# Kernel optimization log

Hardware: AMD Instinct MI355X
Metric: run time of the kernel (lower is better)

## Reference

```python
import jax, jax.numpy as jnp
import numpy as np
import math

NEG_INF = -1000000000.0
D_EMBED = 1024
D_K = 1024
N_HEADS = 16
D_H = D_EMBED // N_HEADS


def setup_inputs() -> dict:
    key = jax.random.key(0)
    ks = jax.random.split(key, 12)
    B, S = 2, 2048
    s = 0.02
    return {
        "embed": jax.random.normal(ks[0], (B, S, D_EMBED), dtype=jnp.float32),
        "key": jax.random.normal(ks[1], (B, S, D_K), dtype=jnp.float32),
        "attn_mask": jax.random.randint(ks[2], (B, S, S), 0, 2, dtype=jnp.int32),
        "Wq": jax.random.normal(ks[3], (D_EMBED, D_EMBED), dtype=jnp.float32) * s,
        "bq": jnp.zeros((D_EMBED,), dtype=jnp.float32),
        "Wk": jax.random.normal(ks[4], (D_EMBED, D_K), dtype=jnp.float32) * s,
        "bk": jnp.zeros((D_EMBED,), dtype=jnp.float32),
        "Wv": jax.random.normal(ks[5], (D_EMBED, D_K), dtype=jnp.float32) * s,
        "bv": jnp.zeros((D_EMBED,), dtype=jnp.float32),
        "Wo": jax.random.normal(ks[6], (D_EMBED, D_EMBED), dtype=jnp.float32) * s,
        "bo": jnp.zeros((D_EMBED,), dtype=jnp.float32),
    }


def _alibi_bias(seq_len: int, n_heads: int) -> jnp.ndarray:
    # symmetric |i-j| distances, slopes 2^-(8k/H) for k=1..H
    r = jnp.arange(seq_len)
    pos = jnp.abs(r[None, :] - r[:, None]).astype(jnp.float32)  # [S, S]
    step = 8.0 / n_heads
    ms = 2.0 ** (-jnp.arange(step, 8.0 + step, step, dtype=jnp.float32))  # [H]
    return ms[:, None, None] * pos[None, :, :]  # [H, S, S]


def reference(embed, key, attn_mask, Wq, bq, Wk, bk, Wv, bv, Wo, bo):
    B, Sq, _ = embed.shape
    Sk = key.shape[1]
    Q = embed @ Wq.T + bq          # [B, Sq, D]
    K = key @ Wk.T + bk            # [B, Sk, D]
    V = key @ Wv.T + bv            # [B, Sk, D]
    Qh = Q.reshape(B, Sq, N_HEADS, D_H).transpose(0, 2, 1, 3)  # [B, H, Sq, d_h]
    Kh = K.reshape(B, Sk, N_HEADS, D_H).transpose(0, 2, 1, 3)
    Vh = V.reshape(B, Sk, N_HEADS, D_H).transpose(0, 2, 1, 3)
    attn = jnp.einsum("bhqd,bhkd->bhqk", Qh, Kh)
    # ALiBi bias subtracted BEFORE scaling (as in source)
    attn = attn - _alibi_bias(Sq, N_HEADS)[None]
    attn = attn * (1.0 / math.sqrt(D_EMBED))  # note: scale uses d_embed, not d_h
    attn = jnp.where(attn_mask[:, None, :, :] == 0, NEG_INF, attn)
    attn = jax.nn.softmax(attn, axis=-1)
    out = jnp.einsum("bhqk,bhkd->bhqd", attn, Vh)
    out = out.transpose(0, 2, 1, 3).reshape(B, Sq, D_EMBED)
    return out @ Wo.T + bo
```

## Files before the change

### kernel.cpp

```cpp
#include <hip/hip_runtime.h>


typedef _Float16 f16;
typedef __attribute__((ext_vector_type(8))) _Float16 f16x8;
typedef __attribute__((ext_vector_type(4))) _Float16 f16x4;
typedef __attribute__((ext_vector_type(4))) float f32x4;
typedef unsigned long long u64;
typedef unsigned int u32;

#define MFMA16 __builtin_amdgcn_mfma_f32_16x16x32_f16
#define MFMA16K16 __builtin_amdgcn_mfma_f32_16x16x16f16

__global__ __launch_bounds__(256) void k_convert(
    const float* __restrict__ embed, const float* __restrict__ key,
    const float* __restrict__ wq, const float* __restrict__ wk,
    const float* __restrict__ wv, const float* __restrict__ wo,
    f16* __restrict__ xe, f16* __restrict__ xk,
    f16* __restrict__ wqh, f16* __restrict__ wkh,
    f16* __restrict__ wvh, f16* __restrict__ woh)
{
    long g = (long)blockIdx.x * 256 + threadIdx.x;
    const float* src; f16* dst; long off;
    if (g < 524288)       { src = embed; dst = xe; off = g; }
    else if (g < 1048576) { src = key;   dst = xk; off = g - 524288; }
    else {
        long t = g - 1048576; int wi = (int)(t >> 17); off = t & 131071;
        if (wi == 0)      { src = wq; dst = wqh; }
        else if (wi == 1) { src = wk; dst = wkh; }
        else if (wi == 2) { src = wv; dst = wvh; }
        else              { src = wo; dst = woh; }
    }
    const float4* s4 = (const float4*)src;
    float4 a = s4[off * 2], b = s4[off * 2 + 1];
    f16x8 o;
    o[0]=(f16)a.x; o[1]=(f16)a.y; o[2]=(f16)a.z; o[3]=(f16)a.w;
    o[4]=(f16)b.x; o[5]=(f16)b.y; o[6]=(f16)b.z; o[7]=(f16)b.w;
    *(f16x8*)(dst + off * 8) = o;
}

__global__ __launch_bounds__(256) void k_packmask(
    const int* __restrict__ mask, u64* __restrict__ bits)
{
    int gw = (blockIdx.x * 256 + threadIdx.x) >> 6;
    int lane = threadIdx.x & 63;
    const int* row = mask + (long)gw * 2048;
    u64* out = bits + (long)gw * 32;
    #pragma unroll 4
    for (int c = 0; c < 32; ++c) {
        int v = row[c * 64 + lane];
        u64 b = __ballot(v != 0);
        if (lane == 0) out[c] = b;
    }
}

__global__ __launch_bounds__(256) void k_qkv(
    const f16* __restrict__ xe, const f16* __restrict__ xk,
    const f16* __restrict__ wqh, const f16* __restrict__ wkh, const f16* __restrict__ wvh,
    const float* __restrict__ bq, const float* __restrict__ bk, const float* __restrict__ bv,
    f16* __restrict__ Qh, f16* __restrict__ Kh, f16* __restrict__ Vt)
{
    int bid = blockIdx.x;
    int which = bid >> 8;
    int rr_ = bid & 255;
    int tm = rr_ >> 3, tn = rr_ & 7;
    const f16* X = (which == 0) ? xe : xk;
    const f16* W = (which == 0) ? wqh : (which == 1) ? wkh : wvh;
    const float* bias = (which == 0) ? bq : (which == 1) ? bk : bv;

    __shared__ f16 smem[128 * 136];
    f16* la = smem;
    f16* lb = smem + 128 * 64;

    int tid = threadIdx.x;
    int lane = tid & 63, wid = tid >> 6;
    int wr = wid >> 1, wc = wid & 1;
    int lm = lane & 15, qd = lane >> 4;

    f32x4 acc[4][4];
    #pragma unroll
    for (int i = 0; i < 4; i++)
        #pragma unroll
        for (int j = 0; j < 4; j++) acc[i][j] = (f32x4)0.0f;

    int m0 = tm * 128, n0 = tn * 128;

    for (int kt = 0; kt < 16; ++kt) {
        int k0 = kt * 64;
        __syncthreads();
        #pragma unroll
        for (int t = 0; t < 4; ++t) {
            int cid = tid + t * 256;
            int row = cid >> 3;
            int cg = cid & 7;
            int sw = cg ^ (row & 7);
            *(f16x8*)&la[row * 64 + sw * 8] =
                *(const f16x8*)&X[(long)(m0 + row) * 1024 + k0 + cg * 8];
            *(f16x8*)&lb[row * 64 + sw * 8] =
                *(const f16x8*)&W[(long)(n0 + row) * 1024 + k0 + cg * 8];
        }
        __syncthreads();
        #pragma unroll
        for (int ks = 0; ks < 2; ++ks) {
            f16x8 af[4], bfr[4];
            #pragma unroll
            for (int i = 0; i < 4; i++) {
                int m = 64 * wr + 16 * i + lm;
                int g = (ks * 4 + qd) ^ (m & 7);
                af[i] = *(const f16x8*)&la[m * 64 + g * 8];
                int n = 64 * wc + 16 * i + lm;
                int g2 = (ks * 4 + qd) ^ (n & 7);
                bfr[i] = *(const f16x8*)&lb[n * 64 + g2 * 8];
            }
            #pragma unroll
            for (int i = 0; i < 4; i++)
                #pragma unroll
                for (int j = 0; j < 4; j++)
                    acc[i][j] = MFMA16(af[i], bfr[j], acc[i][j], 0, 0, 0);
        }
    }

    if (which == 2) {
        #pragma unroll
        for (int j = 0; j < 4; j++) {
            int n = n0 + 64 * wc + 16 * j + lm;
            float bb = bias[n];
            int h = n >> 6, d = n & 63;
            #pragma unroll
            for (int i = 0; i < 4; i++) {
                int mbase = m0 + 64 * wr + 16 * i + 4 * qd;
                f16x4 pk;
                #pragma unroll
                for (int r = 0; r < 4; ++r) pk[r] = (f16)(acc[i][j][r] + bb);
                int b = mbase >> 11, s = mbase & 2047;
                *(f16x4*)&Vt[(((long)(b * 16 + h)) * 64 + d) * 2048 + s] = pk;
            }
        }
    } else {
        f16* dst = (which == 0) ? Qh : Kh;
        float sc = (which == 0) ? 0.0450842252f : 1.0f;
        __syncthreads();
        #pragma unroll
        for (int j = 0; j < 4; j++) {
            int col = 64 * wc + 16 * j + lm;
            float bb = bias[n0 + col];
            #pragma unroll
            for (int i = 0; i < 4; i++) {
                int row = 64 * wr + 16 * i + 4 * qd;
                #pragma unroll
                for (int r = 0; r < 4; ++r)
                    smem[(row + r) * 136 + col] = (f16)((acc[i][j][r] + bb) * sc);
            }
        }
        __syncthreads();
        #pragma unroll
        for (int t = 0; t < 8; ++t) {
            int ci = tid + t * 256;
            int row = ci >> 4, cg = ci & 15;
            f16x8 v = *(const f16x8*)&smem[row * 136 + cg * 8];
            int m = m0 + row;
            int b = m >> 11, s = m & 2047;
            int h = (n0 >> 6) + (cg >> 3);
            int d0 = (cg & 7) * 8;
            *(f16x8*)&dst[(((long)(b * 16 + h)) * 2048 + s) * 64 + d0] = v;
        }
    }
}

__global__ __launch_bounds__(256, 2) void k_attn(
    const f16* __restrict__ Qh, const f16* __restrict__ Kh, const f16* __restrict__ Vt,
    const u64* __restrict__ mbits, f16* __restrict__ O)
{
    int bid = blockIdx.x;
    int qt = bid & 15;
    int h = (bid >> 4) & 15;
    int b = bid >> 8;
    int q0 = qt * 128;

    const f16* Qg = Qh + ((long)(b * 16 + h)) * 2048 * 64;
    const f16* Kg = Kh + ((long)(b * 16 + h)) * 2048 * 64;
    const f16* Vg = Vt + ((long)(b * 16 + h)) * 64 * 2048;

    __shared__ f16 ks[128 * 64];
    __shared__ f16 vs[64 * 128];

    int tid = threadIdx.x, lane = tid & 63, wid = tid >> 6;
    int lm = lane & 15, qd = lane >> 4;

    int qb = q0 + 32 * wid;
    const u64* Mrow0 = mbits + ((long)(b * 2048) + qb + lm) * 32;
    const u64* Mrow1 = mbits + ((long)(b * 2048) + qb + 16 + lm) * 32;

    f16x8 aq[2][2];
    #pragma unroll
    for (int g = 0; g < 2; ++g)
        #pragma unroll
        for (int ksi = 0; ksi < 2; ++ksi)
            aq[g][ksi] = *(const f16x8*)&Qg[(long)(qb + 16 * g + lm) * 64 + ksi * 32 + qd * 8];

    f32x4 oacc[2][4], lacc[2];
    #pragma unroll
    for (int g = 0; g < 2; ++g) {
        #pragma unroll
        for (int c = 0; c < 4; c++) oacc[g][c] = (f32x4)0.0f;
        lacc[g] = (f32x4)0.0f;
    }
    f16x4 vone4;
    #pragma unroll
    for (int j = 0; j < 4; j++) vone4[j] = (f16)1.0f;

    float negc2 = -__builtin_amdgcn_exp2f(-0.5f * (float)(h + 1)) * 0.0450842252f;

    for (int kt = 0; kt < 16; ++kt) {
        int k0 = kt * 128;
        __syncthreads();
        #pragma unroll
        for (int t = 0; t < 4; ++t) {
            int cid = tid + t * 256;
            int row = cid >> 3, cg = cid & 7;
            int sw = cg ^ (row & 7);
            *(f16x8*)&ks[row * 64 + sw * 8] =
                *(const f16x8*)&Kg[(long)(k0 + row) * 64 + cg * 8];
            int vrow = cid >> 4, vg = cid & 15;
            int vsw = vg ^ (vrow & 7);
            *(f16x8*)&vs[vrow * 128 + vsw * 8] =
                *(const f16x8*)&Vg[(long)vrow * 2048 + k0 + vg * 8];
        }
        __syncthreads();

        u64 w0a = Mrow0[kt * 2], w1a = Mrow0[kt * 2 + 1];
        u64 w0b = Mrow1[kt * 2], w1b = Mrow1[kt * 2 + 1];

        f32x4 sacc[2][8];
        #pragma unroll
        for (int g = 0; g < 2; ++g)
            #pragma unroll
            for (int c = 0; c < 8; c++) sacc[g][c] = (f32x4)0.0f;
        #pragma unroll
        for (int ksi = 0; ksi < 2; ++ksi) {
            #pragma unroll
            for (int c = 0; c < 8; c++) {
                int kr = 16 * c + lm;
                int gg = (ksi * 4 + qd) ^ (kr & 7);
                f16x8 ak = *(const f16x8*)&ks[kr * 64 + gg * 8];
                sacc[0][c] = MFMA16(ak, aq[0][ksi], sacc[0][c], 0, 0, 0);
                sacc[1][c] = MFMA16(ak, aq[1][ksi], sacc[1][c], 0, 0, 0);
            }
        }

        float qmk0 = (float)(qb + lm - k0 - 4 * qd);
        float qmk1 = qmk0 + 16.0f;
        int shb = 4 * qd;
        int vgq = qd >> 1;
        int off4 = (qd & 1) * 4;
        #pragma unroll
        for (int c = 0; c < 8; c++) {
            u32 niba = (u32)(((c < 4) ? w0a : w1a) >> (16 * (c & 3) + shb)) & 15u;
            u32 nibb = (u32)(((c < 4) ? w0b : w1b) >> (16 * (c & 3) + shb)) & 15u;
            float qc0 = qmk0 - 16.0f * (float)c;
            float qc1 = qmk1 - 16.0f * (float)c;
            f16x4 pk0, pk1;
            #pragma unroll
            for (int r = 0; r < 4; ++r) {
                float u0 = fmaf(fabsf(qc0 - (float)r), negc2, sacc[0][c][r]);
                u0 = ((niba >> r) & 1u) ? u0 : -1e30f;
                pk0[r] = (f16)__builtin_amdgcn_exp2f(u0);
                float u1 = fmaf(fabsf(qc1 - (float)r), negc2, sacc[1][c][r]);
                u1 = ((nibb >> r) & 1u) ? u1 : -1e30f;
                pk1[r] = (f16)__builtin_amdgcn_exp2f(u1);
            }
            int vgc = 2 * c + vgq;
            #pragma unroll
            for (int cc = 0; cc < 4; ++cc) {
                int d = 16 * cc + lm;
                f16x4 vb = *(const f16x4*)&vs[d * 128 + (vgc ^ (d & 7)) * 8 + off4];
                oacc[0][cc] = MFMA16K16(pk0, vb, oacc[0][cc], 0, 0, 0);
                oacc[1][cc] = MFMA16K16(pk1, vb, oacc[1][cc], 0, 0, 0);
            }
            lacc[0] = MFMA16K16(pk0, vone4, lacc[0], 0, 0, 0);
            lacc[1] = MFMA16K16(pk1, vone4, lacc[1], 0, 0, 0);
        }
    }

    #pragma unroll
    for (int g = 0; g < 2; ++g) {
        #pragma unroll
        for (int r = 0; r < 4; ++r) {
            float linv = 1.0f / fmaxf(lacc[g][r], 1e-30f);
            long rowbase = ((long)(b * 2048 + qb + 16 * g + 4 * qd + r)) * 1024 + h * 64;
            #pragma unroll
            for (int cc = 0; cc < 4; ++cc)
                O[rowbase + 16 * cc + lm] = (f16)(oacc[g][cc][r] * linv);
        }
    }
}

__global__ __launch_bounds__(256) void k_proj(
    const f16* __restrict__ Oh, const f16* __restrict__ woh,
    const float* __restrict__ bo, float* __restrict__ out)
{
    int bid = blockIdx.x;
    int tm = bid >> 3, tn = bid & 7;

    __shared__ f16 la[128 * 64];
    __shared__ f16 lb[128 * 64];

    int tid = threadIdx.x;
    int lane = tid & 63, wid = tid >> 6;
    int wr = wid >> 1, wc = wid & 1;
    int lm = lane & 15, qd = lane >> 4;

    f32x4 acc[4][4];
    #pragma unroll
    for (int i = 0; i < 4; i++)
        #pragma unroll
        for (int j = 0; j < 4; j++) acc[i][j] = (f32x4)0.0f;

    int m0 = tm * 128, n0 = tn * 128;

    for (int kt = 0; kt < 16; ++kt) {
        int k0 = kt * 64;
        __syncthreads();
        #pragma unroll
        for (int t = 0; t < 4; ++t) {
            int cid = tid + t * 256;
            int row = cid >> 3;
            int cg = cid & 7;
            int sw = cg ^ (row & 7);
            *(f16x8*)&la[row * 64 + sw * 8] =
                *(const f16x8*)&Oh[(long)(m0 + row) * 1024 + k0 + cg * 8];
            *(f16x8*)&lb[row * 64 + sw * 8] =
                *(const f16x8*)&woh[(long)(n0 + row) * 1024 + k0 + cg * 8];
        }
        __syncthreads();
        #pragma unroll
        for (int ks = 0; ks < 2; ++ks) {
            f16x8 af[4], bfr[4];
            #pragma unroll
            for (int i = 0; i < 4; i++) {
                int m = 64 * wr + 16 * i + lm;
                int g = (ks * 4 + qd) ^ (m & 7);
                af[i] = *(const f16x8*)&la[m * 64 + g * 8];
                int n = 64 * wc + 16 * i + lm;
                int g2 = (ks * 4 + qd) ^ (n & 7);
                bfr[i] = *(const f16x8*)&lb[n * 64 + g2 * 8];
            }
            #pragma unroll
            for (int i = 0; i < 4; i++)
                #pragma unroll
                for (int j = 0; j < 4; j++)
                    acc[i][j] = MFMA16(af[i], bfr[j], acc[i][j], 0, 0, 0);
        }
    }

    #pragma unroll
    for (int j = 0; j < 4; j++) {
        int n = n0 + 64 * wc + 16 * j + lm;
        float bb = bo[n];
        #pragma unroll
        for (int i = 0; i < 4; i++) {
            int mbase = m0 + 64 * wr + 16 * i + 4 * qd;
            #pragma unroll
            for (int r = 0; r < 4; ++r)
                out[(long)(mbase + r) * 1024 + n] = acc[i][j][r] + bb;
        }
    }
}

extern "C" void kernel_launch(void* const* d_in, const int* in_sizes, int n_in,
                              void* d_out, int out_size, void* d_ws, size_t ws_size,
                              hipStream_t stream)
{
    const float* embed = (const float*)d_in[0];
    const float* key   = (const float*)d_in[1];
    const int*   mask  = (const int*)d_in[2];
    const float* Wq = (const float*)d_in[3];
    const float* bq = (const float*)d_in[4];
    const float* Wk = (const float*)d_in[5];
    const float* bk = (const float*)d_in[6];
    const float* Wv = (const float*)d_in[7];
    const float* bv = (const float*)d_in[8];
    const float* Wo = (const float*)d_in[9];
    const float* bo = (const float*)d_in[10];

    char* ws = (char*)d_ws;
    f16* xe  = (f16*)(ws + 0);
    f16* xk  = (f16*)(ws + 8388608);
    f16* wqh = (f16*)(ws + 16777216);
    f16* wkh = (f16*)(ws + 18874368);
    f16* wvh = (f16*)(ws + 20971520);
    f16* woh = (f16*)(ws + 23068672);
    f16* Qh  = (f16*)(ws + 25165824);
    f16* Kh  = (f16*)(ws + 33554432);
    f16* Vt  = (f16*)(ws + 41943040);
    f16* Oh  = (f16*)(ws + 50331648);
    u64* mb  = (u64*)(ws + 58720256);
    float* out = (float*)d_out;

    k_convert<<<6144, 256, 0, stream>>>(embed, key, Wq, Wk, Wv, Wo,
                                        xe, xk, wqh, wkh, wvh, woh);
    k_packmask<<<1024, 256, 0, stream>>>(mask, mb);
    k_qkv<<<768, 256, 0, stream>>>(xe, xk, wqh, wkh, wvh, bq, bk, bv, Qh, Kh, Vt);
    k_attn<<<512, 256, 0, stream>>>(Qh, Kh, Vt, mb, Oh);
    k_proj<<<256, 256, 0, stream>>>(Oh, woh, bo, out);
}
```

Measured before the change: 287.5 us.

## Split attention keys across two wave groups with direct global-to-LDS loads

After: 287.3 us. No clear change (-0.1%).

```diff
diff --git a/kernel.cpp b/kernel.cpp
--- a/kernel.cpp
+++ b/kernel.cpp
@@ -10,6 +10,13 @@
 
 #define MFMA16 __builtin_amdgcn_mfma_f32_16x16x32_f16
 #define MFMA16K16 __builtin_amdgcn_mfma_f32_16x16x16f16
+
+__device__ __forceinline__ void gl16(const f16* g, f16* l) {
+    __builtin_amdgcn_global_load_lds(
+        (const __attribute__((address_space(1))) void*)(const void*)g,
+        (__attribute__((address_space(3))) void*)(void*)l,
+        16, 0, 0);
+}
 
 __global__ __launch_bounds__(256) void k_convert(
     const float* __restrict__ embed, const float* __restrict__ key,
@@ -166,7 +173,7 @@
     }
 }
 
-__global__ __launch_bounds__(256, 2) void k_attn(
+__global__ __launch_bounds__(512, 4) void k_attn(
     const f16* __restrict__ Qh, const f16* __restrict__ Kh, const f16* __restrict__ Vt,
     const u64* __restrict__ mbits, f16* __restrict__ O)
 {
@@ -180,16 +187,39 @@
     const f16* Kg = Kh + ((long)(b * 16 + h)) * 2048 * 64;
     const f16* Vg = Vt + ((long)(b * 16 + h)) * 64 * 2048;
 
-    __shared__ f16 ks[128 * 64];
-    __shared__ f16 vs[64 * 128];
+    __shared__ f16 smem[32768];
 
     int tid = threadIdx.x, lane = tid & 63, wid = tid >> 6;
     int lm = lane & 15, qd = lane >> 4;
-
-    int qb = q0 + 32 * wid;
+    int qs = wid & 3;
+    int hf = wid >> 2;
+
+    int qb = q0 + 32 * qs;
     const u64* Mrow0 = mbits + ((long)(b * 2048) + qb + lm) * 32;
     const u64* Mrow1 = mbits + ((long)(b * 2048) + qb + 16 + lm) * 32;
 
+    int bi = wid >> 1, sub = wid & 1;
+    f16* ldst = smem + bi * 8192 + sub * 4096;
+    const f16* gE; const f16* gO; long gstep;
+    if (bi < 2) {
+        int krow0 = sub * 64 + (lane >> 3);
+        int kcg = (lane & 7) ^ (krow0 & 7);
+        gE = Kg + ((long)bi * 1024 + krow0) * 64 + kcg * 8;
+        gO = gE + 512;
+        gstep = 1024;
+    } else {
+        int vh = bi - 2;
+        int vrow0 = sub * 32 + (lane >> 4);
+        int vgE = (lane & 15) ^ (vrow0 & 7);
+        gE = Vg + (long)vrow0 * 2048 + vh * 1024 + vgE * 8;
+        gO = Vg + (long)(vrow0 + 4) * 2048 + vh * 1024 + (vgE ^ 4) * 8;
+        gstep = 16384;
+    }
+    long giter = (bi < 2) ? (long)128 * 64 : 128;
+
+    const f16* ksH = smem + hf * 8192;
+    const f16* vsH = smem + 16384 + hf * 8192;
+
     f16x8 aq[2][2];
     #pragma unroll
     for (int g = 0; g < 2; ++g)
@@ -210,50 +240,38 @@
 
     float negc2 = -__builtin_amdgcn_exp2f(-0.5f * (float)(h + 1)) * 0.0450842252f;
 
-    for (int kt = 0; kt < 16; ++kt) {
-        int k0 = kt * 128;
-        __syncthreads();
-        #pragma unroll
-        for (int t = 0; t < 4; ++t) {
-            int cid = tid + t * 256;
-            int row = cid >> 3, cg = cid & 7;
-            int sw = cg ^ (row & 7);
-            *(f16x8*)&ks[row * 64 + sw * 8] =
-                *(const f16x8*)&Kg[(long)(k0 + row) * 64 + cg * 8];
-            int vrow = cid >> 4, vg = cid & 15;
-            int vsw = vg ^ (vrow & 7);
-            *(f16x8*)&vs[vrow * 128 + vsw * 8] =
-                *(const f16x8*)&Vg[(long)vrow * 2048 + k0 + vg * 8];
-        }
-        __syncthreads();
-
+    int vgq = qd >> 1;
+    int off4 = (qd & 1) * 4;
+    int shb = 4 * qd;
+
+    for (int it = 0; it < 8; ++it) {
+        __syncthreads();
+        #pragma unroll
+        for (int p = 0; p < 4; ++p) {
+            gl16(gE + p * gstep, ldst + (2 * p) * 512);
+            gl16(gO + p * gstep, ldst + (2 * p + 1) * 512);
+        }
+        gE += giter; gO += giter;
+        __syncthreads();
+
+        int kt = hf * 8 + it;
         u64 w0a = Mrow0[kt * 2], w1a = Mrow0[kt * 2 + 1];
         u64 w0b = Mrow1[kt * 2], w1b = Mrow1[kt * 2 + 1];
 
-        f32x4 sacc[2][8];
-        #pragma unroll
-        for (int g = 0; g < 2; ++g)
-            #pragma unroll
-            for (int c = 0; c < 8; c++) sacc[g][c] = (f32x4)0.0f;
-        #pragma unroll
-        for (int ksi = 0; ksi < 2; ++ksi) {
-            #pragma unroll
-            for (int c = 0; c < 8; c++) {
-                int kr = 16 * c + lm;
+        float qmk0 = (float)(qb + lm - kt * 128 - 4 * qd);
+        float qmk1 = qmk0 + 16.0f;
+
+        #pragma unroll
+        for (int c = 0; c < 8; ++c) {
+            int kr = 16 * c + lm;
+            f32x4 s0 = (f32x4)0.0f, s1 = (f32x4)0.0f;
+            #pragma unroll
+            for (int ksi = 0; ksi < 2; ++ksi) {
                 int gg = (ksi * 4 + qd) ^ (kr & 7);
-                f16x8 ak = *(const f16x8*)&ks[kr * 64 + gg * 8];
-                sacc[0][c] = MFMA16(ak, aq[0][ksi], sacc[0][c], 0, 0, 0);
-                sacc[1][c] = MFMA16(ak, aq[1][ksi], sacc[1][c], 0, 0, 0);
-            }
-        }
-
-        float qmk0 = (float)(qb + lm - k0 - 4 * qd);
-        float qmk1 = qmk0 + 16.0f;
-        int shb = 4 * qd;
-        int vgq = qd >> 1;
-        int off4 = (qd & 1) * 4;
-        #pragma unroll
-        for (int c = 0; c < 8; c++) {
+                f16x8 ak = *(const f16x8*)&ksH[kr * 64 + gg * 8];
+                s0 = MFMA16(ak, aq[0][ksi], s0, 0, 0, 0);
+                s1 = MFMA16(ak, aq[1][ksi], s1, 0, 0, 0);
+            }
             u32 niba = (u32)(((c < 4) ? w0a : w1a) >> (16 * (c & 3) + shb)) & 15u;
             u32 nibb = (u32)(((c < 4) ? w0b : w1b) >> (16 * (c & 3) + shb)) & 15u;
             float qc0 = qmk0 - 16.0f * (float)c;
@@ -261,10 +279,10 @@
             f16x4 pk0, pk1;
             #pragma unroll
             for (int r = 0; r < 4; ++r) {
-                float u0 = fmaf(fabsf(qc0 - (float)r), negc2, sacc[0][c][r]);
+                float u0 = fmaf(fabsf(qc0 - (float)r), negc2, s0[r]);
                 u0 = ((niba >> r) & 1u) ? u0 : -1e30f;
                 pk0[r] = (f16)__builtin_amdgcn_exp2f(u0);
-                float u1 = fmaf(fabsf(qc1 - (float)r), negc2, sacc[1][c][r]);
+                float u1 = fmaf(fabsf(qc1 - (float)r), negc2, s1[r]);
                 u1 = ((nibb >> r) & 1u) ? u1 : -1e30f;
                 pk1[r] = (f16)__builtin_amdgcn_exp2f(u1);
             }
@@ -272,7 +290,7 @@
             #pragma unroll
             for (int cc = 0; cc < 4; ++cc) {
                 int d = 16 * cc + lm;
-                f16x4 vb = *(const f16x4*)&vs[d * 128 + (vgc ^ (d & 7)) * 8 + off4];
+                f16x4 vb = *(const f16x4*)&vsH[d * 128 + (vgc ^ (d & 7)) * 8 + off4];
                 oacc[0][cc] = MFMA16K16(pk0, vb, oacc[0][cc], 0, 0, 0);
                 oacc[1][cc] = MFMA16K16(pk1, vb, oacc[1][cc], 0, 0, 0);
             }
@@ -281,16 +299,50 @@
         }
     }
 
-    #pragma unroll
-    for (int g = 0; g < 2; ++g) {
-        #pragma unroll
-        for (int r = 0; r < 4; ++r) {
-            float linv = 1.0f / fmaxf(lacc[g][r], 1e-30f);
-            long rowbase = ((long)(b * 2048 + qb + 16 * g + 4 * qd + r)) * 1024 + h * 64;
+    __syncthreads();
+    float* cO = (float*)smem;
+    float* lL = (float*)(smem + 16384);
+    f16*  fO  = smem + 16640;
+
+    if (hf == 1) {
+        #pragma unroll
+        for (int g = 0; g < 2; ++g) {
             #pragma unroll
             for (int cc = 0; cc < 4; ++cc)
-                O[rowbase + 16 * cc + lm] = (f16)(oacc[g][cc][r] * linv);
-        }
+                #pragma unroll
+                for (int r = 0; r < 4; ++r)
+                    cO[(qs * 32 + 16 * g + 4 * qd + r) * 64 + 16 * cc + lm] = oacc[g][cc][r];
+            if (lm == 0) {
+                #pragma unroll
+                for (int r = 0; r < 4; ++r)
+                    lL[qs * 32 + 16 * g + 4 * qd + r] = lacc[g][r];
+            }
+        }
+    }
+    __syncthreads();
+    if (hf == 0) {
+        #pragma unroll
+        for (int g = 0; g < 2; ++g) {
+            float linv[4];
+            #pragma unroll
+            for (int r = 0; r < 4; ++r)
+                linv[r] = 1.0f / fmaxf(lacc[g][r] + lL[qs * 32 + 16 * g + 4 * qd + r], 1e-30f);
+            #pragma unroll
+            for (int cc = 0; cc < 4; ++cc)
+                #pragma unroll
+                for (int r = 0; r < 4; ++r) {
+                    int idx = (qs * 32 + 16 * g + 4 * qd + r) * 64 + 16 * cc + lm;
+                    fO[idx] = (f16)((oacc[g][cc][r] + cO[idx]) * linv[r]);
+                }
+        }
+    }
+    __syncthreads();
+    #pragma unroll
+    for (int t = 0; t < 2; ++t) {
+        int ci = tid + t * 512;
+        int q = ci >> 3, dc = ci & 7;
+        f16x8 v = *(const f16x8*)&fO[q * 64 + dc * 8];
+        *(f16x8*)&O[((long)(b * 2048 + q0 + q)) * 1024 + h * 64 + dc * 8] = v;
     }
 }
 
@@ -400,6 +452,6 @@
                                         xe, xk, wqh, wkh, wvh, woh);
     k_packmask<<<1024, 256, 0, stream>>>(mask, mb);
     k_qkv<<<768, 256, 0, stream>>>(xe, xk, wqh, wkh, wvh, bq, bk, bv, Qh, Kh, Vt);
-    k_attn<<<512, 256, 0, stream>>>(Qh, Kh, Vt, mb, Oh);
+    k_attn<<<512, 512, 0, stream>>>(Qh, Kh, Vt, mb, Oh);
     k_proj<<<256, 256, 0, stream>>>(Oh, woh, bo, out);
 }
```
